# Kernel tuning notes

Hardware: AMD Instinct MI355X
Metric: run time of the kernel (lower is better)

## Reference

```python
import jax, jax.numpy as jnp
import numpy as np

B, N, H = 8, 256, 768
P = 128          # path_hidden_size
HEADS = 12
D = H // HEADS   # 64
EPS = 1e-5


def layer_norm(x, g, b):
    mu = jnp.mean(x, axis=-1, keepdims=True)
    var = jnp.mean((x - mu) ** 2, axis=-1, keepdims=True)
    return (x - mu) * jax.lax.rsqrt(var + EPS) * g + b


def setup_inputs() -> dict:
    key = jax.random.key(0)
    ks = jax.random.split(key, 16)
    s = 0.02
    return {
        "nodes": jax.random.normal(ks[0], (B, N, H), jnp.float32),
        "bias": jax.random.normal(ks[1], (B, HEADS, N, N), jnp.float32),
        "paths": jax.random.normal(ks[2], (B, N, N, P), jnp.float32),
        "Wq": jax.random.normal(ks[3], (H, H), jnp.float32) * s,
        "bq": jnp.zeros((H,), jnp.float32),
        "Wk": jax.random.normal(ks[4], (H, H), jnp.float32) * s,
        "bk": jnp.zeros((H,), jnp.float32),
        "Wv": jax.random.normal(ks[5], (H, H), jnp.float32) * s,
        "bv": jnp.zeros((H,), jnp.float32),
        "Wsk": jax.random.normal(ks[6], (P, D), jnp.float32) * s,
        "bsk": jnp.zeros((D,), jnp.float32),
        "Wsv": jax.random.normal(ks[7], (P, D), jnp.float32) * s,
        "bsv": jnp.zeros((D,), jnp.float32),
        "Wo": jax.random.normal(ks[8], (H, H), jnp.float32) * s,
        "bo": jnp.zeros((H,), jnp.float32),
        "g_path": jnp.ones((P,), jnp.float32),
        "b_path": jnp.zeros((P,), jnp.float32),
        "g_out": jnp.ones((H,), jnp.float32),
        "b_out": jnp.zeros((H,), jnp.float32),
    }


def reference(nodes, bias, paths, Wq, bq, Wk, bk, Wv, bv, Wsk, bsk, Wsv, bsv,
              Wo, bo, g_path, b_path, g_out, b_out):
    # q/k/v: [B,N,H] -> [B,heads,N,D]
    def split(x):
        return x.reshape(B, N, HEADS, D).transpose(0, 2, 1, 3)

    q = split(nodes @ Wq + bq)
    k = split(nodes @ Wk + bk)
    v = split(nodes @ Wv + bv)

    pn = layer_norm(paths, g_path, b_path)          # [B,N,N,P]
    struct_k = pn @ Wsk + bsk                       # [B,N,N,D]
    struct_v = pn @ Wsv + bsv                       # [B,N,N,D]

    q = q * (D ** -0.5)
    # content scores + per-query-row structural scores + bias
    w = (jnp.einsum('bhqd,bhkd->bhqk', q, k)
         + jnp.einsum('bhqd,bqkd->bhqk', q, struct_k)
         + bias)
    w = jax.nn.softmax(w, axis=-1)                  # [B,heads,N,N]

    out = (jnp.einsum('bhqk,bhkd->bhqd', w, v)
           + jnp.einsum('bhqk,bqkd->bhqd', w, struct_v))
    out = out.transpose(0, 2, 1, 3).reshape(B, N, H)  # combine heads
    out = jax.nn.relu(out @ Wo + bo)
    # dropout is identity in eval mode
    return layer_norm(nodes + out, g_out, b_out)
```

## Files before the change

kernel.cpp:

```cpp
#include <hip/hip_runtime.h>
#include <stdint.h>

#define Bb 8
#define Nn 256
#define Hh 768
#define Pp 128
#define HEADS 12
#define Dd 64
#define EPSf 1e-5f

typedef __attribute__((ext_vector_type(8))) short bhalf8;
typedef __attribute__((ext_vector_type(4))) float f32x4;

__device__ __forceinline__ unsigned short f2bf(float f) {
    union { float f; unsigned u; } v; v.f = f;
    unsigned r = v.u + 0x7FFFu + ((v.u >> 16) & 1u);
    return (unsigned short)(r >> 16);
}

__global__ __launch_bounds__(256) void k_transpose4(const float* __restrict__ a0, const float* __restrict__ a1,
                                                    const float* __restrict__ a2, const float* __restrict__ a3,
                                                    unsigned short* __restrict__ o0, unsigned short* __restrict__ o1,
                                                    unsigned short* __restrict__ o2, unsigned short* __restrict__ o3) {
    __shared__ float tile[32][33];
    int z = blockIdx.z;
    const float* in = (z == 0) ? a0 : (z == 1) ? a1 : (z == 2) ? a2 : a3;
    unsigned short* out = (z == 0) ? o0 : (z == 1) ? o1 : (z == 2) ? o2 : o3;
    const int R = 768, C = 768;
    int c0 = blockIdx.x * 32, r0 = blockIdx.y * 32;
    int tx = threadIdx.x & 31, ty = threadIdx.x >> 5;
    for (int i = ty; i < 32; i += 8)
        tile[i][tx] = in[(size_t)(r0 + i) * C + c0 + tx];
    __syncthreads();
    for (int i = ty; i < 32; i += 8)
        out[(size_t)(c0 + i) * R + r0 + tx] = f2bf(tile[tx][i]);
}

__global__ __launch_bounds__(256) void k_transpose_small(const float* __restrict__ a0, const float* __restrict__ a1,
                                                         const float* __restrict__ gp,
                                                         unsigned short* __restrict__ o0, unsigned short* __restrict__ o1) {
    __shared__ float tile[32][33];
    int z = blockIdx.z;
    const float* in = (z == 0) ? a0 : a1;
    unsigned short* out = (z == 0) ? o0 : o1;
    const int R = 128, C = 64;
    int c0 = blockIdx.x * 32, r0 = blockIdx.y * 32;
    int tx = threadIdx.x & 31, ty = threadIdx.x >> 5;
    for (int i = ty; i < 32; i += 8)
        tile[i][tx] = in[(size_t)(r0 + i) * C + c0 + tx];
    __syncthreads();
    float g = gp[r0 + tx];
    for (int i = ty; i < 32; i += 8)
        out[(size_t)(c0 + i) * R + r0 + tx] = f2bf(tile[tx][i] * g);
}

__global__ __launch_bounds__(128) void k_prep_bias(const float* __restrict__ Wsk, const float* __restrict__ Wsv,
                                                   const float* __restrict__ bp,
                                                   const float* __restrict__ bsk, const float* __restrict__ bsv,
                                                   float* __restrict__ bskv2) {
    int d = threadIdx.x;
    const float* W = (d < 64) ? Wsk : Wsv;
    int dd = d & 63;
    float s = (d < 64) ? bsk[dd] : bsv[dd];
    for (int p2 = 0; p2 < 128; p2++) s += bp[p2] * W[p2 * 64 + dd];
    bskv2[d] = s;
}

__global__ __launch_bounds__(256) void k_qkv(const float* __restrict__ nodes,
                                             const unsigned short* __restrict__ Wt,
                                             const float* __restrict__ bq, const float* __restrict__ bk,
                                             const float* __restrict__ bv,
                                             float* __restrict__ qs, float* __restrict__ kk,
                                             float* __restrict__ vv) {
    __shared__ __align__(16) unsigned short Alds[64 * 72];
    __shared__ __align__(16) unsigned short Blds[128 * 72];
    int tid = threadIdx.x;
    int m0 = blockIdx.y * 64;
    int n0 = blockIdx.x * 128;
    int w = tid >> 6, lane = tid & 63;
    int wm = w >> 1, wn = w & 1;
    int lm = lane & 15, lq = lane >> 4;
    f32x4 acc[2][4];
#pragma unroll
    for (int i = 0; i < 2; i++)
#pragma unroll
        for (int j = 0; j < 4; j++) acc[i][j] = (f32x4){0.f, 0.f, 0.f, 0.f};

    for (int kt = 0; kt < 768; kt += 64) {
#pragma unroll
        for (int t = 0; t < 4; t++) {
            int c = t * 256 + tid;
            int row = c >> 4, cc = c & 15;
            float4 v = *(const float4*)(nodes + (size_t)(m0 + row) * 768 + kt + cc * 4);
            uint2 uu;
            uu.x = (unsigned)f2bf(v.x) | ((unsigned)f2bf(v.y) << 16);
            uu.y = (unsigned)f2bf(v.z) | ((unsigned)f2bf(v.w) << 16);
            *(uint2*)(Alds + row * 72 + cc * 4) = uu;
        }
#pragma unroll
        for (int t = 0; t < 4; t++) {
            int c = t * 256 + tid;
            int n = c >> 3, kc = c & 7;
            uint4 v = *(const uint4*)(Wt + (size_t)(n0 + n) * 768 + kt + kc * 8);
            *(uint4*)(Blds + n * 72 + kc * 8) = v;
        }
        __syncthreads();
#pragma unroll
        for (int ks = 0; ks < 2; ks++) {
            bhalf8 af[2];
#pragma unroll
            for (int mi = 0; mi < 2; mi++)
                af[mi] = *(const bhalf8*)(Alds + (wm * 32 + mi * 16 + lm) * 72 + ks * 32 + lq * 8);
#pragma unroll
            for (int nt = 0; nt < 4; nt++) {
                bhalf8 bf = *(const bhalf8*)(Blds + (wn * 64 + nt * 16 + lm) * 72 + ks * 32 + lq * 8);
#pragma unroll
                for (int mi = 0; mi < 2; mi++)
                    acc[mi][nt] = __builtin_amdgcn_mfma_f32_16x16x32_bf16(af[mi], bf, acc[mi][nt], 0, 0, 0);
            }
        }
        __syncthreads();
    }
    int wsel = n0 / 768;
    int nb = n0 % 768;
    const float* bias = (wsel == 0) ? bq : (wsel == 1) ? bk : bv;
    float* dst = (wsel == 0) ? qs : (wsel == 1) ? kk : vv;
    float scale = (wsel == 0) ? 0.125f : 1.0f;
#pragma unroll
    for (int mi = 0; mi < 2; mi++)
#pragma unroll
        for (int nt = 0; nt < 4; nt++)
#pragma unroll
            for (int r = 0; r < 4; r++) {
                int row = m0 + wm * 32 + mi * 16 + lq * 4 + r;
                int col = nb + wn * 64 + nt * 16 + lm;
                int hh = col >> 6, d = col & 63;
                int b = row >> 8, qn = row & 255;
                float val = (acc[mi][nt][r] + bias[col]) * scale;
                dst[(((size_t)b * HEADS + hh) * Nn + qn) * Dd + d] = val;
            }
}

__global__ __launch_bounds__(256) void k_scores(const float* __restrict__ qs,
                                                const float* __restrict__ kk,
                                                const float* __restrict__ bias,
                                                float* __restrict__ wg) {
    __shared__ __align__(16) unsigned short Alds[64 * 72];
    __shared__ __align__(16) unsigned short Blds[64 * 72];
    int tid = threadIdx.x;
    int bh = blockIdx.z;
    int m0 = blockIdx.y * 64;
    int n0 = blockIdx.x * 64;
    int w = tid >> 6, lane = tid & 63, lm = lane & 15, lq = lane >> 4;
    const float* Abase = qs + ((size_t)bh * Nn + m0) * Dd;
    const float* Bbase = kk + ((size_t)bh * Nn + n0) * Dd;
#pragma unroll
    for (int t = 0; t < 4; t++) {
        int c = t * 256 + tid;
        int row = c >> 4, cc = c & 15;
        float4 va = *(const float4*)(Abase + (size_t)row * 64 + cc * 4);
        uint2 ua;
        ua.x = (unsigned)f2bf(va.x) | ((unsigned)f2bf(va.y) << 16);
        ua.y = (unsigned)f2bf(va.z) | ((unsigned)f2bf(va.w) << 16);
        *(uint2*)(Alds + row * 72 + cc * 4) = ua;
        float4 vb = *(const float4*)(Bbase + (size_t)row * 64 + cc * 4);
        uint2 ub;
        ub.x = (unsigned)f2bf(vb.x) | ((unsigned)f2bf(vb.y) << 16);
        ub.y = (unsigned)f2bf(vb.z) | ((unsigned)f2bf(vb.w) << 16);
        *(uint2*)(Blds + row * 72 + cc * 4) = ub;
    }
    __syncthreads();
    f32x4 acc[4];
#pragma unroll
    for (int i = 0; i < 4; i++) acc[i] = (f32x4){0.f, 0.f, 0.f, 0.f};
#pragma unroll
    for (int ks = 0; ks < 2; ks++) {
        bhalf8 af = *(const bhalf8*)(Alds + (w * 16 + lm) * 72 + ks * 32 + lq * 8);
#pragma unroll
        for (int nt = 0; nt < 4; nt++) {
            bhalf8 bf = *(const bhalf8*)(Blds + (nt * 16 + lm) * 72 + ks * 32 + lq * 8);
            acc[nt] = __builtin_amdgcn_mfma_f32_16x16x32_bf16(af, bf, acc[nt], 0, 0, 0);
        }
    }
#pragma unroll
    for (int nt = 0; nt < 4; nt++)
#pragma unroll
        for (int r = 0; r < 4; r++) {
            int row = m0 + w * 16 + lq * 4 + r;
            int col = n0 + nt * 16 + lm;
            size_t idx = ((size_t)bh * Nn + row) * Nn + col;
            wg[idx] = acc[nt][r] + bias[idx];
        }
}

__global__ __launch_bounds__(256, 2) void k_attn(const float* __restrict__ qs,
                                                 const float* __restrict__ paths,
                                                 const unsigned short* __restrict__ Wskvt,
                                                 const float* __restrict__ bskv2,
                                                 float* __restrict__ wg,
                                                 float* __restrict__ attn) {
    __shared__ __align__(16) unsigned short SKbuf[256 * 72];
    __shared__ __align__(16) unsigned short A2[16 * 264];
    __shared__ float redm[64];
    __shared__ float reds[64];
    unsigned short* SVT = SKbuf;

    int tid = threadIdx.x;
    int bq = blockIdx.x;
    int b = bq >> 8, q = bq & 255;
    int w = tid >> 6, lane = tid & 63, lm = lane & 15, lq = lane >> 4;

    bhalf8 af1[2];
    {
        bhalf8 z = (bhalf8){0, 0, 0, 0, 0, 0, 0, 0};
        af1[0] = z; af1[1] = z;
        if (lm < 12) {
            const float* qp = qs + (((size_t)b * HEADS + lm) * Nn + q) * Dd;
#pragma unroll
            for (int ks = 0; ks < 2; ks++) {
                float4 v0 = *(const float4*)(qp + ks * 32 + lq * 8);
                float4 v1 = *(const float4*)(qp + ks * 32 + lq * 8 + 4);
                bhalf8 t;
                t[0] = (short)f2bf(v0.x); t[1] = (short)f2bf(v0.y);
                t[2] = (short)f2bf(v0.z); t[3] = (short)f2bf(v0.w);
                t[4] = (short)f2bf(v1.x); t[5] = (short)f2bf(v1.y);
                t[6] = (short)f2bf(v1.z); t[7] = (short)f2bf(v1.w);
                af1[ks] = t;
            }
        }
    }
    float bv_[8];
#pragma unroll
    for (int nt = 0; nt < 8; nt++) bv_[nt] = bskv2[nt * 16 + lm];

    const float* ppath = paths + (size_t)bq * (256 * 128);
    f32x4 accSV[2][2][4];

#pragma unroll
    for (int p = 0; p < 2; p++) {
        f32x4 acc[2][8];
#pragma unroll
        for (int i = 0; i < 2; i++)
#pragma unroll
            for (int j = 0; j < 8; j++) acc[i][j] = (f32x4){0.f, 0.f, 0.f, 0.f};
        bhalf8 afr[2][4];
#pragma unroll
        for (int mi = 0; mi < 2; mi++) {
            int R = w * 64 + p * 32 + mi * 16 + lm;
            const float* pr = ppath + (size_t)R * 128;
            float x[32];
#pragma unroll
            for (int ks = 0; ks < 4; ks++) {
                float4 a = *(const float4*)(pr + ks * 32 + lq * 8);
                float4 c = *(const float4*)(pr + ks * 32 + lq * 8 + 4);
                x[ks * 8 + 0] = a.x; x[ks * 8 + 1] = a.y; x[ks * 8 + 2] = a.z; x[ks * 8 + 3] = a.w;
                x[ks * 8 + 4] = c.x; x[ks * 8 + 5] = c.y; x[ks * 8 + 6] = c.z; x[ks * 8 + 7] = c.w;
            }
            float s = 0.f, s2 = 0.f;
#pragma unroll
            for (int i = 0; i < 32; i++) { s += x[i]; s2 += x[i] * x[i]; }
            s  += __shfl_xor(s, 16);  s2 += __shfl_xor(s2, 16);
            s  += __shfl_xor(s, 32);  s2 += __shfl_xor(s2, 32);
            float mu = s * (1.f / 128.f);
            float var = s2 * (1.f / 128.f) - mu * mu;
            float rs = rsqrtf(var + EPSf);
#pragma unroll
            for (int ks = 0; ks < 4; ks++) {
                bhalf8 t;
#pragma unroll
                for (int j = 0; j < 8; j++)
                    t[j] = (short)f2bf((x[ks * 8 + j] - mu) * rs);
                afr[mi][ks] = t;
            }
        }
#pragma unroll
        for (int ks = 0; ks < 4; ks++) {
#pragma unroll
            for (int nt = 0; nt < 8; nt++) {
                bhalf8 bf = *(const bhalf8*)(Wskvt + (size_t)(nt * 16 + lm) * 128 + ks * 32 + lq * 8);
#pragma unroll
                for (int mi = 0; mi < 2; mi++)
                    acc[mi][nt] = __builtin_amdgcn_mfma_f32_16x16x32_bf16(afr[mi][ks], bf, acc[mi][nt], 0, 0, 0);
            }
        }
#pragma unroll
        for (int mi = 0; mi < 2; mi++) {
#pragma unroll
            for (int nt = 0; nt < 4; nt++) {
                int col = nt * 16 + lm;
#pragma unroll
                for (int rr = 0; rr < 4; rr++) {
                    int R2 = w * 64 + p * 32 + mi * 16 + lq * 4 + rr;
                    SKbuf[R2 * 72 + col] = f2bf(acc[mi][nt][rr] + bv_[nt]);
                }
            }
#pragma unroll
            for (int nt = 0; nt < 4; nt++) accSV[p][mi][nt] = acc[mi][nt + 4];
        }
    }
    __syncthreads();

    size_t wbase = ((size_t)b * HEADS) * (Nn * Nn) + (size_t)q * Nn;
    float wgv[4][4];
#pragma unroll
    for (int nt = 0; nt < 4; nt++) {
        int col = w * 64 + nt * 16 + lm;
#pragma unroll
        for (int r = 0; r < 4; r++) {
            int row = lq * 4 + r;
            wgv[nt][r] = (row < 12) ? wg[wbase + (size_t)row * (Nn * Nn) + col] : 0.f;
        }
    }
    f32x4 acc1[4];
#pragma unroll
    for (int i = 0; i < 4; i++) acc1[i] = (f32x4){0.f, 0.f, 0.f, 0.f};
#pragma unroll
    for (int ks = 0; ks < 2; ks++) {
#pragma unroll
        for (int nt = 0; nt < 4; nt++) {
            int n0 = w * 64 + nt * 16;
            bhalf8 bf = *(const bhalf8*)(SKbuf + (n0 + lm) * 72 + ks * 32 + lq * 8);
            acc1[nt] = __builtin_amdgcn_mfma_f32_16x16x32_bf16(af1[ks], bf, acc1[nt], 0, 0, 0);
        }
    }
    float S[4][4];
#pragma unroll
    for (int nt = 0; nt < 4; nt++)
#pragma unroll
        for (int r = 0; r < 4; r++) S[nt][r] = acc1[nt][r] + wgv[nt][r];

    __syncthreads();
#pragma unroll
    for (int p = 0; p < 2; p++)
#pragma unroll
        for (int mi = 0; mi < 2; mi++)
#pragma unroll
            for (int nt = 0; nt < 4; nt++) {
                int d = nt * 16 + lm;
#pragma unroll
                for (int rr = 0; rr < 4; rr++) {
                    int R2 = w * 64 + p * 32 + mi * 16 + lq * 4 + rr;
                    SVT[d * 264 + R2] = f2bf(accSV[p][mi][nt][rr] + bv_[nt + 4]);
                }
            }

    float m4[4];
#pragma unroll
    for (int r = 0; r < 4; r++)
        m4[r] = fmaxf(fmaxf(S[0][r], S[1][r]), fmaxf(S[2][r], S[3][r]));
#pragma unroll
    for (int mk = 1; mk < 16; mk <<= 1)
#pragma unroll
        for (int r = 0; r < 4; r++) m4[r] = fmaxf(m4[r], __shfl_xor(m4[r], mk));
    if (lm == 0) {
#pragma unroll
        for (int r = 0; r < 4; r++) redm[(lq * 4 + r) * 4 + w] = m4[r];
    }
    __syncthreads();
    float rowmax[4];
#pragma unroll
    for (int r = 0; r < 4; r++) {
        int row = lq * 4 + r;
        rowmax[r] = fmaxf(fmaxf(redm[row * 4 + 0], redm[row * 4 + 1]),
                          fmaxf(redm[row * 4 + 2], redm[row * 4 + 3]));
    }
    float P[4][4], psum[4];
#pragma unroll
    for (int r = 0; r < 4; r++) {
#pragma unroll
        for (int nt = 0; nt < 4; nt++) P[nt][r] = __expf(S[nt][r] - rowmax[r]);
        psum[r] = (P[0][r] + P[1][r]) + (P[2][r] + P[3][r]);
    }
#pragma unroll
    for (int mk = 1; mk < 16; mk <<= 1)
#pragma unroll
        for (int r = 0; r < 4; r++) psum[r] += __shfl_xor(psum[r], mk);
    if (lm == 0) {
#pragma unroll
        for (int r = 0; r < 4; r++) reds[(lq * 4 + r) * 4 + w] = psum[r];
    }
    __syncthreads();
    float inv[4];
#pragma unroll
    for (int r = 0; r < 4; r++) {
        int row = lq * 4 + r;
        inv[r] = 1.f / (((reds[row * 4 + 0] + reds[row * 4 + 1]) + (reds[row * 4 + 2] + reds[row * 4 + 3])));
    }
#pragma unroll
    for (int nt = 0; nt < 4; nt++)
#pragma unroll
        for (int r = 0; r < 4; r++) {
            int row = lq * 4 + r;
            int col = w * 64 + nt * 16 + lm;
            float pv = P[nt][r] * inv[r];
            A2[row * 264 + col] = f2bf(pv);
            if (row < 12) wg[wbase + (size_t)row * (Nn * Nn) + col] = pv;
        }
    __syncthreads();

    f32x4 acc2 = (f32x4){0.f, 0.f, 0.f, 0.f};
#pragma unroll
    for (int ks = 0; ks < 8; ks++) {
        bhalf8 af = *(const bhalf8*)(A2 + lm * 264 + ks * 32 + lq * 8);
        bhalf8 bf = *(const bhalf8*)(SVT + (w * 16 + lm) * 264 + ks * 32 + lq * 8);
        acc2 = __builtin_amdgcn_mfma_f32_16x16x32_bf16(af, bf, acc2, 0, 0, 0);
    }
#pragma unroll
    for (int r = 0; r < 4; r++) {
        int row = lq * 4 + r;
        if (row < 12) attn[(size_t)bq * Hh + row * 64 + w * 16 + lm] = acc2[r];
    }
}

__global__ __launch_bounds__(256) void k_ctxout(const float* __restrict__ wg,
                                                const float* __restrict__ vv,
                                                float* __restrict__ attn) {
    __shared__ __align__(16) float Al[64 * 68];
    __shared__ __align__(16) float Bl[64 * 68];
    int tid = threadIdx.x;
    int bh = blockIdx.y;
    int m0 = blockIdx.x * 64;
    int b = bh / 12, h = bh % 12;
    int tx = tid & 15, ty = tid >> 4;
    int c0 = tx * 4, r0 = ty * 4;
    float acc[4][4];
#pragma unroll
    for (int i = 0; i < 4; i++)
#pragma unroll
        for (int j = 0; j < 4; j++) acc[i][j] = 0.f;
    const float* Abase = wg + ((size_t)bh * Nn + m0) * Nn;
    const float* Bbase = vv + (size_t)bh * Nn * Dd;
    for (int kt = 0; kt < 256; kt += 64) {
#pragma unroll
        for (int t = 0; t < 4; t++) {
            int c = t * 256 + tid;
            int row = c >> 4, cc = c & 15;
            *(float4*)(Al + row * 68 + cc * 4) = *(const float4*)(Abase + (size_t)row * 256 + kt + cc * 4);
            *(float4*)(Bl + row * 68 + cc * 4) = *(const float4*)(Bbase + (size_t)(kt + row) * 64 + cc * 4);
        }
        __syncthreads();
#pragma unroll 8
        for (int k = 0; k < 64; k++) {
            float4 bv4 = *(const float4*)(Bl + k * 68 + c0);
            float a0 = Al[(r0 + 0) * 68 + k];
            float a1 = Al[(r0 + 1) * 68 + k];
            float a2 = Al[(r0 + 2) * 68 + k];
            float a3 = Al[(r0 + 3) * 68 + k];
            acc[0][0] += a0 * bv4.x; acc[0][1] += a0 * bv4.y; acc[0][2] += a0 * bv4.z; acc[0][3] += a0 * bv4.w;
            acc[1][0] += a1 * bv4.x; acc[1][1] += a1 * bv4.y; acc[1][2] += a1 * bv4.z; acc[1][3] += a1 * bv4.w;
            acc[2][0] += a2 * bv4.x; acc[2][1] += a2 * bv4.y; acc[2][2] += a2 * bv4.z; acc[2][3] += a2 * bv4.w;
            acc[3][0] += a3 * bv4.x; acc[3][1] += a3 * bv4.y; acc[3][2] += a3 * bv4.z; acc[3][3] += a3 * bv4.w;
        }
        __syncthreads();
    }
#pragma unroll
    for (int i = 0; i < 4; i++)
#pragma unroll
        for (int j = 0; j < 4; j++) {
            size_t o = ((size_t)b * Nn + m0 + r0 + i) * Hh + h * 64 + c0 + j;
            attn[o] += acc[i][j];
        }
}

__global__ __launch_bounds__(256) void k_outproj(const float* __restrict__ attn,
                                                 const unsigned short* __restrict__ Wot,
                                                 const float* __restrict__ bo,
                                                 const float* __restrict__ nodes,
                                                 float* __restrict__ tmp) {
    __shared__ __align__(16) unsigned short Alds[64 * 72];
    __shared__ __align__(16) unsigned short Blds[128 * 72];
    int tid = threadIdx.x;
    int m0 = blockIdx.y * 64;
    int n0 = blockIdx.x * 128;
    int w = tid >> 6, lane = tid & 63;
    int wm = w >> 1, wn = w & 1;
    int lm = lane & 15, lq = lane >> 4;
    f32x4 acc[2][4];
#pragma unroll
    for (int i = 0; i < 2; i++)
#pragma unroll
        for (int j = 0; j < 4; j++) acc[i][j] = (f32x4){0.f, 0.f, 0.f, 0.f};
    for (int kt = 0; kt < 768; kt += 64) {
#pragma unroll
        for (int t = 0; t < 4; t++) {
            int c = t * 256 + tid;
            int row = c >> 4, cc = c & 15;
            float4 v = *(const float4*)(attn + (size_t)(m0 + row) * 768 + kt + cc * 4);
            uint2 uu;
            uu.x = (unsigned)f2bf(v.x) | ((unsigned)f2bf(v.y) << 16);
            uu.y = (unsigned)f2bf(v.z) | ((unsigned)f2bf(v.w) << 16);
            *(uint2*)(Alds + row * 72 + cc * 4) = uu;
        }
#pragma unroll
        for (int t = 0; t < 4; t++) {
            int c = t * 256 + tid;
            int n = c >> 3, kc = c & 7;
            uint4 v = *(const uint4*)(Wot + (size_t)(n0 + n) * 768 + kt + kc * 8);
            *(uint4*)(Blds + n * 72 + kc * 8) = v;
        }
        __syncthreads();
#pragma unroll
        for (int ks = 0; ks < 2; ks++) {
            bhalf8 af[2];
#pragma unroll
            for (int mi = 0; mi < 2; mi++)
                af[mi] = *(const bhalf8*)(Alds + (wm * 32 + mi * 16 + lm) * 72 + ks * 32 + lq * 8);
#pragma unroll
            for (int nt = 0; nt < 4; nt++) {
                bhalf8 bf = *(const bhalf8*)(Blds + (wn * 64 + nt * 16 + lm) * 72 + ks * 32 + lq * 8);
#pragma unroll
                for (int mi = 0; mi < 2; mi++)
                    acc[mi][nt] = __builtin_amdgcn_mfma_f32_16x16x32_bf16(af[mi], bf, acc[mi][nt], 0, 0, 0);
            }
        }
        __syncthreads();
    }
#pragma unroll
    for (int mi = 0; mi < 2; mi++)
#pragma unroll
        for (int nt = 0; nt < 4; nt++)
#pragma unroll
            for (int r = 0; r < 4; r++) {
                int row = m0 + wm * 32 + mi * 16 + lq * 4 + r;
                int col = n0 + wn * 64 + nt * 16 + lm;
                float val = acc[mi][nt][r] + bo[col];
                val = fmaxf(val, 0.f) + nodes[(size_t)row * 768 + col];
                tmp[(size_t)row * 768 + col] = val;
            }
}

__global__ __launch_bounds__(256) void k_finalln(const float* __restrict__ tmp,
                                                 const float* __restrict__ go,
                                                 const float* __restrict__ bout,
                                                 float* __restrict__ out) {
    __shared__ float rs1[4], rs2[4];
    int m = blockIdx.x, tid = threadIdx.x;
    int lane = tid & 63, wid = tid >> 6;
    const float* row = tmp + (size_t)m * 768;
    float x0 = row[tid], x1 = row[tid + 256], x2 = row[tid + 512];
    float s = x0 + x1 + x2;
    float s2 = x0 * x0 + x1 * x1 + x2 * x2;
#pragma unroll
    for (int mk = 32; mk; mk >>= 1) {
        s += __shfl_xor(s, mk);
        s2 += __shfl_xor(s2, mk);
    }
    if (lane == 0) { rs1[wid] = s; rs2[wid] = s2; }
    __syncthreads();
    s = rs1[0] + rs1[1] + rs1[2] + rs1[3];
    s2 = rs2[0] + rs2[1] + rs2[2] + rs2[3];
    float mu = s * (1.f / 768.f);
    float var = s2 * (1.f / 768.f) - mu * mu;
    float rstd = rsqrtf(var + EPSf);
    float* orow = out + (size_t)m * 768;
    orow[tid] = (x0 - mu) * rstd * go[tid] + bout[tid];
    orow[tid + 256] = (x1 - mu) * rstd * go[tid + 256] + bout[tid + 256];
    orow[tid + 512] = (x2 - mu) * rstd * go[tid + 512] + bout[tid + 512];
}

extern "C" void kernel_launch(void* const* d_in, const int* in_sizes, int n_in,
                              void* d_out, int out_size, void* d_ws, size_t ws_size,
                              hipStream_t stream) {
    const float* nodes = (const float*)d_in[0];
    const float* bias  = (const float*)d_in[1];
    const float* paths = (const float*)d_in[2];
    const float* Wq = (const float*)d_in[3];  const float* bq  = (const float*)d_in[4];
    const float* Wk = (const float*)d_in[5];  const float* bk  = (const float*)d_in[6];
    const float* Wv = (const float*)d_in[7];  const float* bv  = (const float*)d_in[8];
    const float* Wsk = (const float*)d_in[9]; const float* bsk = (const float*)d_in[10];
    const float* Wsv = (const float*)d_in[11];const float* bsv = (const float*)d_in[12];
    const float* Wo = (const float*)d_in[13]; const float* bo  = (const float*)d_in[14];
    const float* gp = (const float*)d_in[15]; const float* bp  = (const float*)d_in[16];
    const float* go = (const float*)d_in[17]; const float* bout= (const float*)d_in[18];
    float* out = (float*)d_out;

    char* ws = (char*)d_ws;
    size_t off = 0;
    auto carve = [&](size_t bytes) -> char* {
        char* p = ws + off;
        off += (bytes + 255) & ~(size_t)255;
        return p;
    };
    float* qs   = (float*)carve((size_t)Bb * HEADS * Nn * Dd * 4);
    float* kk   = (float*)carve((size_t)Bb * HEADS * Nn * Dd * 4);
    float* vv   = (float*)carve((size_t)Bb * HEADS * Nn * Dd * 4);
    float* wg   = (float*)carve((size_t)Bb * HEADS * Nn * Nn * 4);
    float* attn = (float*)carve((size_t)Bb * Nn * Hh * 4);
    float* tmp  = (float*)carve((size_t)Bb * Nn * Hh * 4);
    unsigned short* Wqkvt = (unsigned short*)carve((size_t)3 * 768 * 768 * 2);
    unsigned short* Wot   = (unsigned short*)carve((size_t)768 * 768 * 2);
    unsigned short* Wskvt = (unsigned short*)carve((size_t)128 * 128 * 2);
    float* bskv2 = (float*)carve(128 * 4);
    (void)ws_size; (void)in_sizes; (void)n_in; (void)out_size;

    hipLaunchKernelGGL(k_transpose4, dim3(24, 24, 4), dim3(256), 0, stream,
                       Wq, Wk, Wv, Wo,
                       Wqkvt, Wqkvt + (size_t)768 * 768, Wqkvt + (size_t)2 * 768 * 768, Wot);
    hipLaunchKernelGGL(k_transpose_small, dim3(2, 4, 2), dim3(256), 0, stream,
                       Wsk, Wsv, gp, Wskvt, Wskvt + (size_t)64 * 128);
    hipLaunchKernelGGL(k_prep_bias, dim3(1), dim3(128), 0, stream,
                       Wsk, Wsv, bp, bsk, bsv, bskv2);

    hipLaunchKernelGGL(k_qkv, dim3(18, 32), dim3(256), 0, stream, nodes, Wqkvt, bq, bk, bv, qs, kk, vv);
    hipLaunchKernelGGL(k_scores, dim3(4, 4, 96), dim3(256), 0, stream, qs, kk, bias, wg);
    hipLaunchKernelGGL(k_attn, dim3(2048), dim3(256), 0, stream, qs, paths, Wskvt, bskv2, wg, attn);
    hipLaunchKernelGGL(k_ctxout, dim3(4, 96), dim3(256), 0, stream, wg, vv, attn);
    hipLaunchKernelGGL(k_outproj, dim3(6, 32), dim3(256), 0, stream, attn, Wot, bo, nodes, tmp);
    hipLaunchKernelGGL(k_finalln, dim3(2048), dim3(256), 0, stream, tmp, go, bout, out);
}
```

Before: 562.1 us.

## Use bf16 MFMA for context matmul, widen attention block to 512 threads

```diff
diff --git a/kernel.cpp b/kernel.cpp
--- a/kernel.cpp
+++ b/kernel.cpp
@@ -71,7 +71,7 @@
                                              const float* __restrict__ bq, const float* __restrict__ bk,
                                              const float* __restrict__ bv,
                                              float* __restrict__ qs, float* __restrict__ kk,
-                                             float* __restrict__ vv) {
+                                             unsigned short* __restrict__ vt) {
     __shared__ __align__(16) unsigned short Alds[64 * 72];
     __shared__ __align__(16) unsigned short Blds[128 * 72];
     int tid = threadIdx.x;
@@ -123,22 +123,38 @@
     }
     int wsel = n0 / 768;
     int nb = n0 % 768;
-    const float* bias = (wsel == 0) ? bq : (wsel == 1) ? bk : bv;
-    float* dst = (wsel == 0) ? qs : (wsel == 1) ? kk : vv;
-    float scale = (wsel == 0) ? 0.125f : 1.0f;
-#pragma unroll
-    for (int mi = 0; mi < 2; mi++)
-#pragma unroll
-        for (int nt = 0; nt < 4; nt++)
-#pragma unroll
-            for (int r = 0; r < 4; r++) {
-                int row = m0 + wm * 32 + mi * 16 + lq * 4 + r;
-                int col = nb + wn * 64 + nt * 16 + lm;
-                int hh = col >> 6, d = col & 63;
-                int b = row >> 8, qn = row & 255;
-                float val = (acc[mi][nt][r] + bias[col]) * scale;
-                dst[(((size_t)b * HEADS + hh) * Nn + qn) * Dd + d] = val;
-            }
+    if (wsel == 2) {
+#pragma unroll
+        for (int mi = 0; mi < 2; mi++)
+#pragma unroll
+            for (int nt = 0; nt < 4; nt++)
+#pragma unroll
+                for (int r = 0; r < 4; r++) {
+                    int row = m0 + wm * 32 + mi * 16 + lq * 4 + r;
+                    int col = nb + wn * 64 + nt * 16 + lm;
+                    int hh = col >> 6, d = col & 63;
+                    int b = row >> 8, qn = row & 255;
+                    float val = acc[mi][nt][r] + bv[col];
+                    vt[(((size_t)b * HEADS + hh) * Dd + d) * Nn + qn] = f2bf(val);
+                }
+    } else {
+        const float* bias = (wsel == 0) ? bq : bk;
+        float* dst = (wsel == 0) ? qs : kk;
+        float scale = (wsel == 0) ? 0.125f : 1.0f;
+#pragma unroll
+        for (int mi = 0; mi < 2; mi++)
+#pragma unroll
+            for (int nt = 0; nt < 4; nt++)
+#pragma unroll
+                for (int r = 0; r < 4; r++) {
+                    int row = m0 + wm * 32 + mi * 16 + lq * 4 + r;
+                    int col = nb + wn * 64 + nt * 16 + lm;
+                    int hh = col >> 6, d = col & 63;
+                    int b = row >> 8, qn = row & 255;
+                    float val = (acc[mi][nt][r] + bias[col]) * scale;
+                    dst[(((size_t)b * HEADS + hh) * Nn + qn) * Dd + d] = val;
+                }
+    }
 }
 
 __global__ __launch_bounds__(256) void k_scores(const float* __restrict__ qs,
@@ -193,16 +209,17 @@
         }
 }
 
-__global__ __launch_bounds__(256, 2) void k_attn(const float* __restrict__ qs,
+__global__ __launch_bounds__(512, 4) void k_attn(const float* __restrict__ qs,
                                                  const float* __restrict__ paths,
                                                  const unsigned short* __restrict__ Wskvt,
                                                  const float* __restrict__ bskv2,
-                                                 float* __restrict__ wg,
+                                                 const float* __restrict__ wg,
+                                                 unsigned short* __restrict__ wgbf,
                                                  float* __restrict__ attn) {
     __shared__ __align__(16) unsigned short SKbuf[256 * 72];
     __shared__ __align__(16) unsigned short A2[16 * 264];
-    __shared__ float redm[64];
-    __shared__ float reds[64];
+    __shared__ float redm[16 * 8];
+    __shared__ float reds[16 * 8];
     unsigned short* SVT = SKbuf;
 
     int tid = threadIdx.x;
@@ -234,10 +251,9 @@
     for (int nt = 0; nt < 8; nt++) bv_[nt] = bskv2[nt * 16 + lm];
 
     const float* ppath = paths + (size_t)bq * (256 * 128);
-    f32x4 accSV[2][2][4];
-
-#pragma unroll
-    for (int p = 0; p < 2; p++) {
+    f32x4 accSV[2][4];
+
+    {
         f32x4 acc[2][8];
 #pragma unroll
         for (int i = 0; i < 2; i++)
@@ -246,7 +262,7 @@
         bhalf8 afr[2][4];
 #pragma unroll
         for (int mi = 0; mi < 2; mi++) {
-            int R = w * 64 + p * 32 + mi * 16 + lm;
+            int R = w * 32 + mi * 16 + lm;
             const float* pr = ppath + (size_t)R * 128;
             float x[32];
 #pragma unroll
@@ -290,86 +306,85 @@
                 int col = nt * 16 + lm;
 #pragma unroll
                 for (int rr = 0; rr < 4; rr++) {
-                    int R2 = w * 64 + p * 32 + mi * 16 + lq * 4 + rr;
+                    int R2 = w * 32 + mi * 16 + lq * 4 + rr;
                     SKbuf[R2 * 72 + col] = f2bf(acc[mi][nt][rr] + bv_[nt]);
                 }
             }
 #pragma unroll
-            for (int nt = 0; nt < 4; nt++) accSV[p][mi][nt] = acc[mi][nt + 4];
+            for (int nt = 0; nt < 4; nt++) accSV[mi][nt] = acc[mi][nt + 4];
         }
     }
     __syncthreads();
 
     size_t wbase = ((size_t)b * HEADS) * (Nn * Nn) + (size_t)q * Nn;
-    float wgv[4][4];
-#pragma unroll
-    for (int nt = 0; nt < 4; nt++) {
-        int col = w * 64 + nt * 16 + lm;
+    float wgv[2][4];
+#pragma unroll
+    for (int nt = 0; nt < 2; nt++) {
+        int col = w * 32 + nt * 16 + lm;
 #pragma unroll
         for (int r = 0; r < 4; r++) {
             int row = lq * 4 + r;
             wgv[nt][r] = (row < 12) ? wg[wbase + (size_t)row * (Nn * Nn) + col] : 0.f;
         }
     }
-    f32x4 acc1[4];
-#pragma unroll
-    for (int i = 0; i < 4; i++) acc1[i] = (f32x4){0.f, 0.f, 0.f, 0.f};
+    f32x4 acc1[2];
+#pragma unroll
+    for (int i = 0; i < 2; i++) acc1[i] = (f32x4){0.f, 0.f, 0.f, 0.f};
 #pragma unroll
     for (int ks = 0; ks < 2; ks++) {
 #pragma unroll
-        for (int nt = 0; nt < 4; nt++) {
-            int n0 = w * 64 + nt * 16;
+        for (int nt = 0; nt < 2; nt++) {
+            int n0 = w * 32 + nt * 16;
             bhalf8 bf = *(const bhalf8*)(SKbuf + (n0 + lm) * 72 + ks * 32 + lq * 8);
             acc1[nt] = __builtin_amdgcn_mfma_f32_16x16x32_bf16(af1[ks], bf, acc1[nt], 0, 0, 0);
         }
     }
-    float S[4][4];
-#pragma unroll
-    for (int nt = 0; nt < 4; nt++)
+    float S[2][4];
+#pragma unroll
+    for (int nt = 0; nt < 2; nt++)
 #pragma unroll
         for (int r = 0; r < 4; r++) S[nt][r] = acc1[nt][r] + wgv[nt][r];
 
     __syncthreads();
 #pragma unroll
-    for (int p = 0; p < 2; p++)
-#pragma unroll
-        for (int mi = 0; mi < 2; mi++)
-#pragma unroll
-            for (int nt = 0; nt < 4; nt++) {
-                int d = nt * 16 + lm;
-#pragma unroll
-                for (int rr = 0; rr < 4; rr++) {
-                    int R2 = w * 64 + p * 32 + mi * 16 + lq * 4 + rr;
-                    SVT[d * 264 + R2] = f2bf(accSV[p][mi][nt][rr] + bv_[nt + 4]);
-                }
-            }
+    for (int mi = 0; mi < 2; mi++)
+#pragma unroll
+        for (int nt = 0; nt < 4; nt++) {
+            int d = nt * 16 + lm;
+#pragma unroll
+            for (int rr = 0; rr < 4; rr++) {
+                int R2 = w * 32 + mi * 16 + lq * 4 + rr;
+                SVT[d * 264 + R2] = f2bf(accSV[mi][nt][rr] + bv_[nt + 4]);
+            }
+        }
 
     float m4[4];
 #pragma unroll
     for (int r = 0; r < 4; r++)
-        m4[r] = fmaxf(fmaxf(S[0][r], S[1][r]), fmaxf(S[2][r], S[3][r]));
+        m4[r] = fmaxf(S[0][r], S[1][r]);
 #pragma unroll
     for (int mk = 1; mk < 16; mk <<= 1)
 #pragma unroll
         for (int r = 0; r < 4; r++) m4[r] = fmaxf(m4[r], __shfl_xor(m4[r], mk));
     if (lm == 0) {
 #pragma unroll
-        for (int r = 0; r < 4; r++) redm[(lq * 4 + r) * 4 + w] = m4[r];
+        for (int r = 0; r < 4; r++) redm[(lq * 4 + r) * 8 + w] = m4[r];
     }
     __syncthreads();
     float rowmax[4];
 #pragma unroll
     for (int r = 0; r < 4; r++) {
         int row = lq * 4 + r;
-        rowmax[r] = fmaxf(fmaxf(redm[row * 4 + 0], redm[row * 4 + 1]),
-                          fmaxf(redm[row * 4 + 2], redm[row * 4 + 3]));
-    }
-    float P[4][4], psum[4];
+        float a = fmaxf(fmaxf(redm[row * 8 + 0], redm[row * 8 + 1]), fmaxf(redm[row * 8 + 2], redm[row * 8 + 3]));
+        float c = fmaxf(fmaxf(redm[row * 8 + 4], redm[row * 8 + 5]), fmaxf(redm[row * 8 + 6], redm[row * 8 + 7]));
+        rowmax[r] = fmaxf(a, c);
+    }
+    float P[2][4], psum[4];
 #pragma unroll
     for (int r = 0; r < 4; r++) {
 #pragma unroll
-        for (int nt = 0; nt < 4; nt++) P[nt][r] = __expf(S[nt][r] - rowmax[r]);
-        psum[r] = (P[0][r] + P[1][r]) + (P[2][r] + P[3][r]);
+        for (int nt = 0; nt < 2; nt++) P[nt][r] = __expf(S[nt][r] - rowmax[r]);
+        psum[r] = P[0][r] + P[1][r];
     }
 #pragma unroll
     for (int mk = 1; mk < 16; mk <<= 1)
@@ -377,88 +392,89 @@
         for (int r = 0; r < 4; r++) psum[r] += __shfl_xor(psum[r], mk);
     if (lm == 0) {
 #pragma unroll
-        for (int r = 0; r < 4; r++) reds[(lq * 4 + r) * 4 + w] = psum[r];
+        for (int r = 0; r < 4; r++) reds[(lq * 4 + r) * 8 + w] = psum[r];
     }
     __syncthreads();
     float inv[4];
 #pragma unroll
     for (int r = 0; r < 4; r++) {
         int row = lq * 4 + r;
-        inv[r] = 1.f / (((reds[row * 4 + 0] + reds[row * 4 + 1]) + (reds[row * 4 + 2] + reds[row * 4 + 3])));
-    }
-#pragma unroll
-    for (int nt = 0; nt < 4; nt++)
+        float a = (reds[row * 8 + 0] + reds[row * 8 + 1]) + (reds[row * 8 + 2] + reds[row * 8 + 3]);
+        float c = (reds[row * 8 + 4] + reds[row * 8 + 5]) + (reds[row * 8 + 6] + reds[row * 8 + 7]);
+        inv[r] = 1.f / (a + c);
+    }
+#pragma unroll
+    for (int nt = 0; nt < 2; nt++)
 #pragma unroll
         for (int r = 0; r < 4; r++) {
             int row = lq * 4 + r;
-            int col = w * 64 + nt * 16 + lm;
+            int col = w * 32 + nt * 16 + lm;
             float pv = P[nt][r] * inv[r];
-            A2[row * 264 + col] = f2bf(pv);
-            if (row < 12) wg[wbase + (size_t)row * (Nn * Nn) + col] = pv;
-        }
-    __syncthreads();
-
-    f32x4 acc2 = (f32x4){0.f, 0.f, 0.f, 0.f};
-#pragma unroll
-    for (int ks = 0; ks < 8; ks++) {
-        bhalf8 af = *(const bhalf8*)(A2 + lm * 264 + ks * 32 + lq * 8);
-        bhalf8 bf = *(const bhalf8*)(SVT + (w * 16 + lm) * 264 + ks * 32 + lq * 8);
-        acc2 = __builtin_amdgcn_mfma_f32_16x16x32_bf16(af, bf, acc2, 0, 0, 0);
-    }
-#pragma unroll
-    for (int r = 0; r < 4; r++) {
-        int row = lq * 4 + r;
-        if (row < 12) attn[(size_t)bq * Hh + row * 64 + w * 16 + lm] = acc2[r];
-    }
-}
-
-__global__ __launch_bounds__(256) void k_ctxout(const float* __restrict__ wg,
-                                                const float* __restrict__ vv,
+            unsigned short pb = f2bf(pv);
+            A2[row * 264 + col] = pb;
+            if (row < 12) wgbf[wbase + (size_t)row * (Nn * Nn) + col] = pb;
+        }
+    __syncthreads();
+
+    if (w < 4) {
+        f32x4 acc2 = (f32x4){0.f, 0.f, 0.f, 0.f};
+#pragma unroll
+        for (int ks = 0; ks < 8; ks++) {
+            bhalf8 af = *(const bhalf8*)(A2 + lm * 264 + ks * 32 + lq * 8);
+            bhalf8 bf = *(const bhalf8*)(SVT + (w * 16 + lm) * 264 + ks * 32 + lq * 8);
+            acc2 = __builtin_amdgcn_mfma_f32_16x16x32_bf16(af, bf, acc2, 0, 0, 0);
+        }
+#pragma unroll
+        for (int r = 0; r < 4; r++) {
+            int row = lq * 4 + r;
+            if (row < 12) attn[(size_t)bq * Hh + row * 64 + w * 16 + lm] = acc2[r];
+        }
+    }
+}
+
+__global__ __launch_bounds__(256) void k_ctxout(const unsigned short* __restrict__ wgbf,
+                                                const unsigned short* __restrict__ vt,
                                                 float* __restrict__ attn) {
-    __shared__ __align__(16) float Al[64 * 68];
-    __shared__ __align__(16) float Bl[64 * 68];
+    __shared__ __align__(16) unsigned short Alds[64 * 72];
+    __shared__ __align__(16) unsigned short Blds[64 * 72];
     int tid = threadIdx.x;
     int bh = blockIdx.y;
     int m0 = blockIdx.x * 64;
     int b = bh / 12, h = bh % 12;
-    int tx = tid & 15, ty = tid >> 4;
-    int c0 = tx * 4, r0 = ty * 4;
-    float acc[4][4];
-#pragma unroll
-    for (int i = 0; i < 4; i++)
-#pragma unroll
-        for (int j = 0; j < 4; j++) acc[i][j] = 0.f;
-    const float* Abase = wg + ((size_t)bh * Nn + m0) * Nn;
-    const float* Bbase = vv + (size_t)bh * Nn * Dd;
+    int w = tid >> 6, lane = tid & 63, lm = lane & 15, lq = lane >> 4;
+    f32x4 acc[4];
+#pragma unroll
+    for (int i = 0; i < 4; i++) acc[i] = (f32x4){0.f, 0.f, 0.f, 0.f};
+    const unsigned short* Abase = wgbf + ((size_t)bh * Nn + m0) * Nn;
+    const unsigned short* Bbase = vt + (size_t)bh * Dd * Nn;
     for (int kt = 0; kt < 256; kt += 64) {
 #pragma unroll
-        for (int t = 0; t < 4; t++) {
+        for (int t = 0; t < 2; t++) {
             int c = t * 256 + tid;
-            int row = c >> 4, cc = c & 15;
-            *(float4*)(Al + row * 68 + cc * 4) = *(const float4*)(Abase + (size_t)row * 256 + kt + cc * 4);
-            *(float4*)(Bl + row * 68 + cc * 4) = *(const float4*)(Bbase + (size_t)(kt + row) * 64 + cc * 4);
+            int row = c >> 3, kc = c & 7;
+            *(uint4*)(Alds + row * 72 + kc * 8) = *(const uint4*)(Abase + (size_t)row * Nn + kt + kc * 8);
+            *(uint4*)(Blds + row * 72 + kc * 8) = *(const uint4*)(Bbase + (size_t)row * Nn + kt + kc * 8);
         }
         __syncthreads();
-#pragma unroll 8
-        for (int k = 0; k < 64; k++) {
-            float4 bv4 = *(const float4*)(Bl + k * 68 + c0);
-            float a0 = Al[(r0 + 0) * 68 + k];
-            float a1 = Al[(r0 + 1) * 68 + k];
-            float a2 = Al[(r0 + 2) * 68 + k];
-            float a3 = Al[(r0 + 3) * 68 + k];
-            acc[0][0] += a0 * bv4.x; acc[0][1] += a0 * bv4.y; acc[0][2] += a0 * bv4.z; acc[0][3] += a0 * bv4.w;
-            acc[1][0] += a1 * bv4.x; acc[1][1] += a1 * bv4.y; acc[1][2] += a1 * bv4.z; acc[1][3] += a1 * bv4.w;
-            acc[2][0] += a2 * bv4.x; acc[2][1] += a2 * bv4.y; acc[2][2] += a2 * bv4.z; acc[2][3] += a2 * bv4.w;
-            acc[3][0] += a3 * bv4.x; acc[3][1] += a3 * bv4.y; acc[3][2] += a3 * bv4.z; acc[3][3] += a3 * bv4.w;
+#pragma unroll
+        for (int ks = 0; ks < 2; ks++) {
+            bhalf8 af = *(const bhalf8*)(Alds + (w * 16 + lm) * 72 + ks * 32 + lq * 8);
+#pragma unroll
+            for (int nt = 0; nt < 4; nt++) {
+                bhalf8 bf = *(const bhalf8*)(Blds + (nt * 16 + lm) * 72 + ks * 32 + lq * 8);
+                acc[nt] = __builtin_amdgcn_mfma_f32_16x16x32_bf16(af, bf, acc[nt], 0, 0, 0);
+            }
         }
         __syncthreads();
     }
 #pragma unroll
-    for (int i = 0; i < 4; i++)
-#pragma unroll
-        for (int j = 0; j < 4; j++) {
-            size_t o = ((size_t)b * Nn + m0 + r0 + i) * Hh + h * 64 + c0 + j;
-            attn[o] += acc[i][j];
+    for (int nt = 0; nt < 4; nt++)
+#pragma unroll
+        for (int r = 0; r < 4; r++) {
+            int row = m0 + w * 16 + lq * 4 + r;
+            int col = nt * 16 + lm;
+            size_t o = ((size_t)b * Nn + row) * Hh + h * 64 + col;
+            attn[o] += acc[nt][r];
         }
 }
 
@@ -583,8 +599,9 @@
     };
     float* qs   = (float*)carve((size_t)Bb * HEADS * Nn * Dd * 4);
     float* kk   = (float*)carve((size_t)Bb * HEADS * Nn * Dd * 4);
-    float* vv   = (float*)carve((size_t)Bb * HEADS * Nn * Dd * 4);
+    unsigned short* vt = (unsigned short*)carve((size_t)Bb * HEADS * Dd * Nn * 2);
     float* wg   = (float*)carve((size_t)Bb * HEADS * Nn * Nn * 4);
+    unsigned short* wgbf = (unsigned short*)carve((size_t)Bb * HEADS * Nn * Nn * 2);
     float* attn = (float*)carve((size_t)Bb * Nn * Hh * 4);
     float* tmp  = (float*)carve((size_t)Bb * Nn * Hh * 4);
     unsigned short* Wqkvt = (unsigned short*)carve((size_t)3 * 768 * 768 * 2);
@@ -601,10 +618,10 @@
     hipLaunchKernelGGL(k_prep_bias, dim3(1), dim3(128), 0, stream,
                        Wsk, Wsv, bp, bsk, bsv, bskv2);
 
-    hipLaunchKernelGGL(k_qkv, dim3(18, 32), dim3(256), 0, stream, nodes, Wqkvt, bq, bk, bv, qs, kk, vv);
+    hipLaunchKernelGGL(k_qkv, dim3(18, 32), dim3(256), 0, stream, nodes, Wqkvt, bq, bk, bv, qs, kk, vt);
     hipLaunchKernelGGL(k_scores, dim3(4, 4, 96), dim3(256), 0, stream, qs, kk, bias, wg);
-    hipLaunchKernelGGL(k_attn, dim3(2048), dim3(256), 0, stream, qs, paths, Wskvt, bskv2, wg, attn);
-    hipLaunchKernelGGL(k_ctxout, dim3(4, 96), dim3(256), 0, stream, wg, vv, attn);
+    hipLaunchKernelGGL(k_attn, dim3(2048), dim3(512), 0, stream, qs, paths, Wskvt, bskv2, wg, wgbf, attn);
+    hipLaunchKernelGGL(k_ctxout, dim3(4, 96), dim3(256), 0, stream, wgbf, vt, attn);
     hipLaunchKernelGGL(k_outproj, dim3(6, 32), dim3(256), 0, stream, attn, Wot, bo, nodes, tmp);
     hipLaunchKernelGGL(k_finalln, dim3(2048), dim3(256), 0, stream, tmp, go, bout, out);
 }
```

Result: slower. 619.7 us (+10.3%).
